# Performance work log

Measured on AMD Instinct MI355X. Metric: run time of the kernel, lower is better.

Reference implementation:

```python
import jax, jax.numpy as jnp
import numpy as np

# Static architecture constants (from init_kwargs)
NUM_AREAS = 4
E_PER = 512          # excitatory units per area
I_PER = 128          # inhibitory units per area
H = NUM_AREAS * (E_PER + I_PER)   # 2560 hidden units
E_SIZE = NUM_AREAS * E_PER        # 2048 = int(0.8 * H)
NUM_OBJS = 2
IN_UNITS = 64
IN_SIZE = NUM_OBJS * IN_UNITS     # 128
ALPHA = 0.02 / 0.1                # dt_x / tau_x


def _build_masks():
    # Recurrent block-connectivity: tridiagonal area graph (adjacent areas connected)
    rec = np.eye(NUM_AREAS) + np.eye(NUM_AREAS, k=1) + np.eye(NUM_AREAS, k=-1)
    ee = np.kron(rec, np.ones((E_PER, E_PER)))
    ie = np.kron(rec, np.ones((I_PER, E_PER)))
    ei = np.kron(np.eye(NUM_AREAS), np.ones((E_PER, I_PER)))
    ii = np.kron(np.eye(NUM_AREAS), np.ones((I_PER, I_PER)))
    conn_rec = np.block([[ee, ei], [ie, ii]])  # rows/cols ordered [all-E | all-I]
    # Dale sign mask: first E_SIZE columns excitatory (+1), rest inhibitory (-1)
    sign = np.concatenate([np.ones(E_SIZE), -np.ones(H - E_SIZE)])[None, :]
    mask_rec = conn_rec * sign
    np.fill_diagonal(mask_rec, 0.0)  # remove_diag=True in h2h EILinear
    # Input connectivity: only area 0 receives external input (e_prop=1 -> all +1)
    in_mask = np.zeros((NUM_AREAS, NUM_OBJS)); in_mask[0, :] = 1.0
    in_e = np.kron(in_mask, np.ones((E_PER, IN_UNITS)))
    in_i = np.kron(in_mask, np.ones((I_PER, IN_UNITS)))
    mask_in = np.vstack([in_e, in_i])
    return jnp.asarray(mask_rec, jnp.float32), jnp.asarray(mask_in, jnp.float32)

MASK_REC, MASK_IN = _build_masks()


def retanh(x):
    return jnp.tanh(jax.nn.relu(x))


def setup_inputs() -> dict:
    key = jax.random.key(0)
    k1, k2, k3 = jax.random.split(key, 3)
    T, B = 32, 64
    x = jax.random.normal(k1, (T, B, IN_SIZE), dtype=jnp.float32)
    # positive-ish inits (original uses gamma; scale ~ 1/sqrt(fan-in))
    W_in = jax.random.uniform(k2, (H, IN_SIZE), dtype=jnp.float32) * 0.02
    W_rec = jax.random.uniform(k3, (H, H), dtype=jnp.float32) * (1.0 / np.sqrt(H))
    b_rec = jnp.zeros((H,), jnp.float32)
    state0 = jnp.zeros((B, H), jnp.float32)
    return {"x": x, "W_in": W_in, "W_rec": W_rec, "b_rec": b_rec, "state0": state0}


def reference(x, W_in, W_rec, b_rec, state0):
    # Effective weights: pos_function='abs' applied to raw weights, then sign/conn mask
    Wr = jnp.abs(W_rec) * MASK_REC          # [H, H]
    Wi = jnp.abs(W_in) * MASK_IN            # [H, IN_SIZE]

    def step(state, xt):
        out = retanh(state)                                # activation of old state
        total = out @ Wr.T + jax.nn.relu(xt) @ Wi.T + b_rec  # h2h(output) + x2h(relu(x)) + bias
        new_state = state * (1.0 - ALPHA) + ALPHA * total    # leaky integration (sigma=0)
        return new_state, retanh(new_state)

    _, outputs = jax.lax.scan(step, state0, x)  # outputs: [T, B, H]
    return outputs
```

## Files before the change

### kernel.cpp

```cpp
#include <hip/hip_runtime.h>
#include <math.h>

#define HH   2560
#define ESZ  2048
#define BB   64
#define TT   32
#define INSZ 128
constexpr float ALPHA_C = 0.2f;

typedef unsigned short ushort_t;
typedef __attribute__((ext_vector_type(8))) unsigned short u16x8;
typedef __attribute__((ext_vector_type(4))) float f32x4;

__device__ __forceinline__ float retanh_f(float v) { return tanhf(fmaxf(v, 0.f)); }
__device__ __forceinline__ ushort_t f2bf(float f) {
    unsigned u = __float_as_uint(f);
    return (ushort_t)((u + 0x7fffu + ((u >> 16) & 1u)) >> 16);
}

__device__ __forceinline__ int area_ne(int a)  { return (a == 1 || a == 2) ? 1536 : 1024; }
__device__ __forceinline__ int area_elo(int a) { return (a > 0 ? a - 1 : 0) << 9; }

__device__ __forceinline__ void act_store(ushort_t* actF, int a, int p, int b, ushort_t v) {
    int kc = p >> 5, kk = p & 31;
    int lane = ((kk >> 3) << 4) + (b & 15);
    actF[(((a * 52 + kc) << 2) + (b >> 4)) * 512 + lane * 8 + (kk & 7)] = v;
}
__device__ __forceinline__ void scatter_act(ushort_t* actF, int h, int b, ushort_t v) {
    if (h < ESZ) {
        int ae = h >> 9;
        int alo = ae > 0 ? ae - 1 : 0, ahi = ae < 3 ? ae + 1 : 3;
        for (int a = alo; a <= ahi; a++) act_store(actF, a, h - area_elo(a), b, v);
    } else {
        int ai = (h - ESZ) >> 7;
        act_store(actF, ai, area_ne(ai) + (h - (ESZ + (ai << 7))), b, v);
    }
}

__global__ __launch_bounds__(256) void pack_all(
    const float* __restrict__ Wrec, const float* __restrict__ Win,
    const float* __restrict__ x, const float* __restrict__ state0,
    ushort_t* __restrict__ WF, ushort_t* __restrict__ xF,
    float* __restrict__ stateT, ushort_t* __restrict__ actF)
{
    const int bid = blockIdx.x;
    if (bid < 2080) {
        int idx = bid * 256 + threadIdx.x;
        int l = idx & 63;
        int t = idx >> 6;
        int kc = t % 52, mt = t / 52;
        int area = mt / 40, local = mt - area * 40;
        int ridx = local * 16 + (l & 15);
        int h = (ridx < 512) ? ((area << 9) + ridx) : (ESZ + (area << 7) + (ridx - 512));
        int p0 = kc * 32 + ((l >> 4) << 3);
        int ne = area_ne(area), elo = area_elo(area);
        int nrec = ne + 128;
        int ntot = nrec + (area == 0 ? 128 : 0);
        u16x8 o;
#pragma unroll
        for (int j = 0; j < 8; j++) {
            int p = p0 + j;
            float w = 0.f;
            if (p < ne)        { int c = elo + p;                      w = (c == h) ? 0.f :  fabsf(Wrec[(size_t)h * HH + c]); }
            else if (p < nrec) { int c = ESZ + (area << 7) + (p - ne); w = (c == h) ? 0.f : -fabsf(Wrec[(size_t)h * HH + c]); }
            else if (p < ntot) { w = fabsf(Win[(size_t)h * INSZ + (p - nrec)]); }
            o[j] = f2bf(w);
        }
        *(u16x8*)(WF + ((size_t)t * 512 + l * 8)) = o;
    } else if (bid < 3104) {
        int idx = (bid - 2080) * 256 + threadIdx.x;
        int j = idx & 7, l = (idx >> 3) & 63;
        int nt = (idx >> 9) & 3, kc = (idx >> 11) & 3, t = idx >> 13;
        int b = nt * 16 + (l & 15);
        int k = kc * 32 + ((l >> 4) << 3) + j;
        xF[idx] = f2bf(fmaxf(x[((size_t)t * BB + b) * INSZ + k], 0.f));
    } else {
        int idx = (bid - 3104) * 256 + threadIdx.x;
        int b = idx / HH, h = idx - b * HH;
        float s = state0[idx];
        int r = (h < ESZ) ? ((h >> 9) * 640 + (h & 511))
                          : (((h - ESZ) >> 7) * 640 + 512 + ((h - ESZ) & 127));
        stateT[r * BB + b] = s;
        scatter_act(actF, h, b, f2bf(retanh_f(s)));
    }
}

__global__ __launch_bounds__(256) void step9(
    const ushort_t* __restrict__ WF,
    const ushort_t* __restrict__ actF_in,
    ushort_t* __restrict__ actF_out,
    const ushort_t* __restrict__ xFt,
    const float* __restrict__ brec,
    float* __restrict__ stateT,
    float* __restrict__ out_t)
{
    __shared__ float part[4 * 256];
    const int tid = threadIdx.x, lane = tid & 63, wv = tid >> 6;
    const int bid = blockIdx.x;
    const int area = (bid >> 1) & 3;
    const int nt   = ((bid >> 2) & 2) | (bid & 1);
    const int ml   = bid >> 4;
    const int mt   = area * 40 + ml;
    const int r0   = area * 640 + ml * 16;

    f32x4 acc = {0.f, 0.f, 0.f, 0.f};
    const ushort_t* aptr = WF + ((size_t)mt * 52 + wv) * 512 + lane * 8;
    const ushort_t* bptr = actF_in + (((size_t)area * 52 + wv) * 4 + nt) * 512 + lane * 8;
    const ushort_t* xptr = xFt + ((wv * 4) + nt) * 512 + lane * 8;

#define KLOOP(NIT, HASX)                                                     \
    {                                                                        \
        u16x8 af[NIT], bf[NIT];                                              \
        _Pragma("unroll")                                                    \
        for (int i = 0; i < (NIT); i++) {                                    \
            af[i] = *(const u16x8*)(aptr + (size_t)i * 2048);                \
            bf[i] = ((HASX) && i == (NIT) - 1)                               \
                        ? *(const u16x8*)xptr                                \
                        : *(const u16x8*)(bptr + (size_t)i * 8192);          \
        }                                                                    \
        _Pragma("unroll")                                                    \
        for (int i = 0; i < (NIT); i++)                                      \
            asm volatile("v_mfma_f32_16x16x32_bf16 %0, %1, %2, %0"           \
                         : "+v"(acc) : "v"(af[i]), "v"(bf[i]));              \
    }

    if (area == 0)      KLOOP(10, true)
    else if (area == 3) KLOOP(9,  false)
    else                KLOOP(13, false)
#undef KLOOP

    asm volatile("s_nop 7\n\ts_nop 7" : "+v"(acc));

#pragma unroll
    for (int i = 0; i < 4; i++)
        part[wv * 256 + (lane & 15) * 16 + ((lane >> 4) << 2) + i] = acc[i];
    __syncthreads();

    {
        const int mm = tid & 15, nn = tid >> 4;
        float s = part[nn * 16 + mm] + part[256 + nn * 16 + mm]
                + part[512 + nn * 16 + mm] + part[768 + nn * 16 + mm];
        const int b = nt * 16 + nn;
        const int ridx = ml * 16 + mm;
        const int h = (ridx < 512) ? ((area << 9) + ridx)
                                   : (ESZ + (area << 7) + (ridx - 512));
        const int r = r0 + mm;
        float st = stateT[r * BB + b];
        float ns = st * (1.f - ALPHA_C) + ALPHA_C * (s + brec[h]);
        stateT[r * BB + b] = ns;
        float o = retanh_f(ns);
        out_t[(size_t)b * HH + h] = o;
        scatter_act(actF_out, h, b, f2bf(o));
    }
}

__device__ __forceinline__ void area_params(int area, int& e_lo, int& n_e,
                                            int& i_lo, int& n_rec, int& n_tot) {
    e_lo = (area > 0 ? area - 1 : 0) << 9;
    int e_hi = ((area < 3 ? area + 1 : 3) + 1) << 9;
    n_e = e_hi - e_lo;
    i_lo = ESZ + (area << 7);
    n_rec = n_e + 128;
    n_tot = n_rec + (area == 0 ? INSZ : 0);
}
__device__ __forceinline__ int row_h(int area, int idx) {
    return (idx < 512) ? ((area << 9) + idx) : (ESZ + (area << 7) + (idx - 512));
}
__global__ __launch_bounds__(256) void init_state2(const float* __restrict__ state0,
                                                   float* __restrict__ stateT,
                                                   float* __restrict__ act0) {
    int idx = blockIdx.x * 256 + threadIdx.x;
    int b = idx / HH, h = idx - b * HH;
    float s = state0[idx];
    int r = (h < ESZ) ? ((h >> 9) * 640 + (h & 511))
                      : (((h - ESZ) >> 7) * 640 + 512 + ((h - ESZ) & 127));
    stateT[r * BB + b] = s;
    act0[((h >> 1) << 7) + b * 2 + (h & 1)] = retanh_f(s);
}
__global__ __launch_bounds__(1024, 4) void step_raw(
    const float* __restrict__ W, const float* __restrict__ Win,
    const float* __restrict__ brec, const float* __restrict__ x_t,
    const float* __restrict__ actIn, float* __restrict__ actOut,
    float* __restrict__ stateT, float* __restrict__ out_t)
{
    __shared__ float part[16 * 680];
    const int tid = threadIdx.x, lane = tid & 63, wv = tid >> 6;
    const int area = blockIdx.x >> 6;
    const int rb = (blockIdx.x & 63) * 10;
    int e_lo, n_e, i_lo, n_rec, n_tot;
    area_params(area, e_lo, n_e, i_lo, n_rec, n_tot);
    const int r0 = area * 640 + rb;
    const int C = n_tot >> 4;
    float2 acc[10];
#pragma unroll
    for (int j = 0; j < 10; j++) acc[j] = make_float2(0.f, 0.f);
    for (int c = wv; c < C; c += 16) {
        const int p0 = c << 4;
        float2 av[8];
        int cbase;
        if (p0 < n_rec) {
            cbase = (p0 < n_e) ? (e_lo + p0) : (i_lo + (p0 - n_e));
            const float* ap = actIn + ((cbase >> 1) << 7) + lane * 2;
#pragma unroll
            for (int i = 0; i < 8; i++) av[i] = *(const float2*)(ap + (i << 7));
        } else {
            cbase = -1;
            const int k0 = p0 - n_rec;
            const float4* xp = (const float4*)(x_t + lane * INSZ + k0);
#pragma unroll
            for (int q = 0; q < 4; q++) {
                float4 v = xp[q];
                av[2 * q]     = make_float2(fmaxf(v.x, 0.f), fmaxf(v.y, 0.f));
                av[2 * q + 1] = make_float2(fmaxf(v.z, 0.f), fmaxf(v.w, 0.f));
            }
        }
#pragma unroll
        for (int j = 0; j < 10; j++) {
            const int h = row_h(area, rb + j);
            const float sgn = (cbase >= 0 && p0 >= n_e) ? -1.f : 1.f;
            const float* wr = (cbase >= 0) ? (W + (size_t)h * HH + cbase)
                                           : (Win + (size_t)h * INSZ + (p0 - n_rec));
#pragma unroll
            for (int i = 0; i < 8; i++) {
                acc[j].x = fmaf(sgn * fabsf(wr[2 * i]),     av[i].x, acc[j].x);
                acc[j].y = fmaf(sgn * fabsf(wr[2 * i + 1]), av[i].y, acc[j].y);
            }
        }
    }
#pragma unroll
    for (int j = 0; j < 10; j++)
        part[wv * 680 + j * 68 + lane] = acc[j].x + acc[j].y;
    __syncthreads();
    int j = -1, b = 0;
    if (tid < 512)      { b = tid >> 3;      j = tid & 7; }
    else if (tid < 640) { int u = tid - 512; b = u >> 1;  j = 8 + (u & 1); }
    if (j >= 0) {
        const int h = row_h(area, rb + j);
        float s = 0.f;
#pragma unroll
        for (int w16 = 0; w16 < 16; w16++) s += part[w16 * 680 + j * 68 + b];
        float sgn = (h < ESZ) ? 1.f : -1.f;
        s -= sgn * fabsf(W[(size_t)h * HH + h]) * actIn[((h >> 1) << 7) + b * 2 + (h & 1)];
        const int r = r0 + j;
        float st = stateT[r * BB + b];
        float ns = st * (1.f - ALPHA_C) + ALPHA_C * (s + brec[h]);
        stateT[r * BB + b] = ns;
        float o = retanh_f(ns);
        out_t[(size_t)b * HH + h] = o;
        actOut[((h >> 1) << 7) + b * 2 + (h & 1)] = o;
    }
}

extern "C" void kernel_launch(void* const* d_in, const int* in_sizes, int n_in,
                              void* d_out, int out_size, void* d_ws, size_t ws_size,
                              hipStream_t stream) {
    const float* x      = (const float*)d_in[0];
    const float* W_in   = (const float*)d_in[1];
    const float* W_rec  = (const float*)d_in[2];
    const float* b_rec  = (const float*)d_in[3];
    const float* state0 = (const float*)d_in[4];
    float* out = (float*)d_out;

    const size_t WFn = (size_t)160 * 52 * 512;
    const size_t xFn = (size_t)TT * 8192;
    const size_t aFn = (size_t)4 * 52 * 4 * 512;
    const size_t need = (WFn + xFn + 2 * aFn) * 2 + (size_t)HH * BB * 4;

    if (ws_size >= need) {
        ushort_t* WF   = (ushort_t*)d_ws;
        ushort_t* xF   = WF + WFn;
        ushort_t* actA = xF + xFn;
        ushort_t* actB = actA + aFn;
        float* stateT  = (float*)(actB + aFn);

        pack_all<<<3744, 256, 0, stream>>>(W_rec, W_in, x, state0, WF, xF, stateT, actA);
        for (int t = 0; t < TT; t++) {
            ushort_t* ai = (t & 1) ? actB : actA;
            ushort_t* ao = (t & 1) ? actA : actB;
            step9<<<640, 256, 0, stream>>>(WF, ai, ao, xF + (size_t)t * 8192,
                                           b_rec, stateT, out + (size_t)t * BB * HH);
        }
    } else {
        float* ws = (float*)d_ws;
        const size_t bufElems = (size_t)HH * BB;
        float* stateT = ws;
        float* actA   = stateT + bufElems;
        float* actB   = actA + bufElems;
        init_state2<<<(BB * HH) / 256, 256, 0, stream>>>(state0, stateT, actA);
        for (int t = 0; t < TT; t++) {
            const float* ai = (t & 1) ? actB : actA;
            float* ao       = (t & 1) ? actA : actB;
            step_raw<<<256, 1024, 0, stream>>>(W_rec, W_in, b_rec,
                                               x + (size_t)t * BB * INSZ,
                                               ai, ao, stateT, out + (size_t)t * BB * HH);
        }
    }
}
```

Before: 276.7 us.

## Coalesce weight packing reads and split MFMA accumulation into two chains

The weight-packing branch now maps threads to contiguous runs of eight source columns per row, so each thread reads eight consecutive floats from W_rec or W_in instead of gathering strided elements, and it scatters the packed bf16 vector into the MFMA fragment layout. Threads past the used width of a row are skipped. In the step kernel, the MFMA chain alternates between two accumulators that are summed at the end, which shortens the dependent-MFMA latency chain. The packing change alters which threads write which WF entries, so any WF positions not covered by an active thread must already be zero.

Result: no change. 277.0 us (median of 2 runs) (+0.1%).

```diff
diff --git a/kernel.cpp b/kernel.cpp
--- a/kernel.cpp
+++ b/kernel.cpp
@@ -46,27 +46,45 @@
     const int bid = blockIdx.x;
     if (bid < 2080) {
         int idx = bid * 256 + threadIdx.x;
-        int l = idx & 63;
-        int t = idx >> 6;
-        int kc = t % 52, mt = t / 52;
-        int area = mt / 40, local = mt - area * 40;
-        int ridx = local * 16 + (l & 15);
-        int h = (ridx < 512) ? ((area << 9) + ridx) : (ESZ + (area << 7) + (ridx - 512));
-        int p0 = kc * 32 + ((l >> 4) << 3);
-        int ne = area_ne(area), elo = area_elo(area);
+        int h = idx / 208, cc = idx - h * 208;
+        int ar, ridx;
+        if (h < ESZ) { ar = h >> 9;         ridx = h & 511; }
+        else         { ar = (h - ESZ) >> 7; ridx = 512 + ((h - ESZ) & 127); }
+        int ne = area_ne(ar), elo = area_elo(ar);
         int nrec = ne + 128;
-        int ntot = nrec + (area == 0 ? 128 : 0);
-        u16x8 o;
-#pragma unroll
-        for (int j = 0; j < 8; j++) {
-            int p = p0 + j;
-            float w = 0.f;
-            if (p < ne)        { int c = elo + p;                      w = (c == h) ? 0.f :  fabsf(Wrec[(size_t)h * HH + c]); }
-            else if (p < nrec) { int c = ESZ + (area << 7) + (p - ne); w = (c == h) ? 0.f : -fabsf(Wrec[(size_t)h * HH + c]); }
-            else if (p < ntot) { w = fabsf(Win[(size_t)h * INSZ + (p - nrec)]); }
-            o[j] = f2bf(w);
-        }
-        *(u16x8*)(WF + ((size_t)t * 512 + l * 8)) = o;
+        int ntot = nrec + (ar == 0 ? 128 : 0);
+        int p0 = cc * 8;
+        if (p0 < ntot) {
+            float vals[8];
+            if (p0 < ne) {
+                int c0 = elo + p0;
+                const float* src = Wrec + (size_t)h * HH + c0;
+#pragma unroll
+                for (int i = 0; i < 8; i++) {
+                    float w = fabsf(src[i]);
+                    vals[i] = (c0 + i == h) ? 0.f : w;
+                }
+            } else if (p0 < nrec) {
+                int c0 = ESZ + (ar << 7) + (p0 - ne);
+                const float* src = Wrec + (size_t)h * HH + c0;
+#pragma unroll
+                for (int i = 0; i < 8; i++) {
+                    float w = -fabsf(src[i]);
+                    vals[i] = (c0 + i == h) ? 0.f : w;
+                }
+            } else {
+                const float* src = Win + (size_t)h * INSZ + (p0 - nrec);
+#pragma unroll
+                for (int i = 0; i < 8; i++) vals[i] = fabsf(src[i]);
+            }
+            int mt = ar * 40 + (ridx >> 4);
+            int kc = p0 >> 5;
+            int lane = (((p0 >> 3) & 3) << 4) + (ridx & 15);
+            u16x8 o;
+#pragma unroll
+            for (int i = 0; i < 8; i++) o[i] = f2bf(vals[i]);
+            *(u16x8*)(WF + ((size_t)(mt * 52 + kc) * 512 + lane * 8)) = o;
+        }
     } else if (bid < 3104) {
         int idx = (bid - 2080) * 256 + threadIdx.x;
         int j = idx & 7, l = (idx >> 3) & 63;
@@ -103,7 +121,7 @@
     const int mt   = area * 40 + ml;
     const int r0   = area * 640 + ml * 16;
 
-    f32x4 acc = {0.f, 0.f, 0.f, 0.f};
+    f32x4 acc0 = {0.f, 0.f, 0.f, 0.f}, acc1 = {0.f, 0.f, 0.f, 0.f};
     const ushort_t* aptr = WF + ((size_t)mt * 52 + wv) * 512 + lane * 8;
     const ushort_t* bptr = actF_in + (((size_t)area * 52 + wv) * 4 + nt) * 512 + lane * 8;
     const ushort_t* xptr = xFt + ((wv * 4) + nt) * 512 + lane * 8;
@@ -119,9 +137,14 @@
                         : *(const u16x8*)(bptr + (size_t)i * 8192);          \
         }                                                                    \
         _Pragma("unroll")                                                    \
-        for (int i = 0; i < (NIT); i++)                                      \
-            asm volatile("v_mfma_f32_16x16x32_bf16 %0, %1, %2, %0"           \
-                         : "+v"(acc) : "v"(af[i]), "v"(bf[i]));              \
+        for (int i = 0; i < (NIT); i++) {                                    \
+            if (i & 1)                                                       \
+                asm volatile("v_mfma_f32_16x16x32_bf16 %0, %1, %2, %0"       \
+                             : "+v"(acc1) : "v"(af[i]), "v"(bf[i]));         \
+            else                                                             \
+                asm volatile("v_mfma_f32_16x16x32_bf16 %0, %1, %2, %0"       \
+                             : "+v"(acc0) : "v"(af[i]), "v"(bf[i]));         \
+        }                                                                    \
     }
 
     if (area == 0)      KLOOP(10, true)
@@ -129,11 +152,11 @@
     else                KLOOP(13, false)
 #undef KLOOP
 
-    asm volatile("s_nop 7\n\ts_nop 7" : "+v"(acc));
+    asm volatile("s_nop 7\n\ts_nop 7" : "+v"(acc0), "+v"(acc1));
 
 #pragma unroll
     for (int i = 0; i < 4; i++)
-        part[wv * 256 + (lane & 15) * 16 + ((lane >> 4) << 2) + i] = acc[i];
+        part[wv * 256 + (lane & 15) * 16 + ((lane >> 4) << 2) + i] = acc0[i] + acc1[i];
     __syncthreads();
 
     {
```
